# Kernel optimization log

Measured on AMD Instinct MI355X. Metric: run time of the kernel, lower is better.

Reference implementation:

```python
import jax, jax.numpy as jnp
import numpy as np

TAU = 0.2        # temperature
LAM = 0.5        # lambda_weight
P = 128          # proj_dim


def l2n(x):
    # tf.math.l2_normalize semantics: x / sqrt(max(sum(x^2), eps))
    return x / jnp.sqrt(jnp.maximum(jnp.sum(x * x, axis=-1, keepdims=True), 1e-12))


def global_head(feat, W1, b1, W2, b2):
    # GlobalAveragePooling2D -> Dense(2048, relu) -> Dense(128); dropout is identity in eval
    g = jnp.mean(feat, axis=(1, 2))                       # [B, C]
    return jax.nn.relu(g @ W1 + b1) @ W2 + b2             # [B, 128]


def dense_head(feat, W1, b1, W2, b2):
    # 1x1 Conv2D(2048, relu) -> 1x1 Conv2D(128) == per-pixel matmuls
    h = jax.nn.relu(jnp.einsum('bhwc,cd->bhwd', feat, W1) + b1)
    return jnp.einsum('bhwd,de->bhwe', h, W2) + b2        # [B, H, W, 128]


def dense_correspondence(q, k):
    b, h, w, c = q.shape
    f1 = q.reshape(b, h * w, c)
    f2 = k.reshape(b, h * w, c)
    sim = jnp.einsum('bnc,bmc->bnm', f1, f2)              # [B, hw, hw]
    idx = jnp.argmax(sim, axis=-1)                        # [B, hw]
    return jnp.take_along_axis(f2, idx[:, :, None], axis=1)  # batched gather


def info_nce(q, k):
    logits = (q @ k.T) / TAU                              # [N, N]
    lse = jax.nn.logsumexp(logits, axis=-1)
    pos = jnp.diagonal(logits)                            # labels = arange(N)
    return jnp.mean(lse - pos)


def queue_info_nce(q, k, queue):
    l_pos = jnp.sum(q * k, axis=-1, keepdims=True)        # [B, 1]
    l_neg = q @ queue.T                                   # [B, Q]
    logits = jnp.concatenate([l_pos, l_neg], axis=1) / TAU
    # labels are all zero -> positive logit is column 0
    return jnp.mean(jax.nn.logsumexp(logits, axis=-1) - logits[:, 0])


def setup_inputs() -> dict:
    key = jax.random.key(0)
    ks = jax.random.split(key, 16)
    B, H, W, C, D = 8, 28, 28, 1024, 2048
    Q = 65536
    s1 = 0.02
    inp = {
        'feat_q': jax.random.normal(ks[0], (B, H, W, C), jnp.float32),
        'feat_k': jax.random.normal(ks[1], (B, H, W, C), jnp.float32),
        'Wg1': jax.random.normal(ks[2], (C, D), jnp.float32) * s1,
        'bg1': jnp.zeros((D,), jnp.float32),
        'Wg2': jax.random.normal(ks[3], (D, P), jnp.float32) * s1,
        'bg2': jnp.zeros((P,), jnp.float32),
        'Wd1': jax.random.normal(ks[4], (C, D), jnp.float32) * s1,
        'bd1': jnp.zeros((D,), jnp.float32),
        'Wd2': jax.random.normal(ks[5], (D, P), jnp.float32) * s1,
        'bd2': jnp.zeros((P,), jnp.float32),
        'mWg1': jax.random.normal(ks[6], (C, D), jnp.float32) * s1,
        'mbg1': jnp.zeros((D,), jnp.float32),
        'mWg2': jax.random.normal(ks[7], (D, P), jnp.float32) * s1,
        'mbg2': jnp.zeros((P,), jnp.float32),
        'mWd1': jax.random.normal(ks[8], (C, D), jnp.float32) * s1,
        'mbd1': jnp.zeros((D,), jnp.float32),
        'mWd2': jax.random.normal(ks[9], (D, P), jnp.float32) * s1,
        'mbd2': jnp.zeros((P,), jnp.float32),
        'queue': l2n(jax.random.normal(ks[10], (Q, P), jnp.float32)),
    }
    return inp


def reference(feat_q, feat_k, Wg1, bg1, Wg2, bg2, Wd1, bd1, Wd2, bd2,
              mWg1, mbg1, mWg2, mbg2, mWd1, mbd1, mWd2, mbd2, queue):
    # student branch
    q_g = l2n(global_head(feat_q, Wg1, bg1, Wg2, bg2))
    q_d = l2n(dense_head(feat_q, Wd1, bd1, Wd2, bd2))
    # momentum (teacher) branch, stop-gradient as in train_step
    k_g = jax.lax.stop_gradient(l2n(global_head(feat_k, mWg1, mbg1, mWg2, mbg2)))
    k_d = jax.lax.stop_gradient(l2n(dense_head(feat_k, mWd1, mbd1, mWd2, mbd2)))
    # post-warmup path (warmup_epochs=0)
    l_g = queue_info_nce(q_g, k_g, queue)
    matched_k = dense_correspondence(q_d, k_d)
    l_d = info_nce(q_d.reshape(-1, P), matched_k.reshape(-1, P))
    total = (1.0 - LAM) * l_g + LAM * l_d
    return total
```

## Files before the change

kernel.cpp:

```cpp
#include <hip/hip_runtime.h>
#include <cstdint>

#define TAU_INV 5.0f
#define L2E 1.4426950408889634f

using ushort = unsigned short;
typedef __attribute__((ext_vector_type(8))) short s16x8;
typedef __attribute__((ext_vector_type(4))) float f32x4;

static __device__ __forceinline__ ushort f2bf(float x) {
  unsigned u = __float_as_uint(x);
  return (ushort)((u + 0x7fffu + ((u >> 16) & 1u)) >> 16);
}

static __device__ __forceinline__ float fexp2(float x) {
#if __has_builtin(__builtin_amdgcn_exp2f)
  return __builtin_amdgcn_exp2f(x);
#else
  return exp2f(x);
#endif
}

static __device__ __forceinline__ void gload_lds16(const void* g, void* l) {
  __builtin_amdgcn_global_load_lds(
      reinterpret_cast<const __attribute__((address_space(1))) void*>(
          reinterpret_cast<uintptr_t>(g)),
      reinterpret_cast<__attribute__((address_space(3))) void*>(
          (unsigned)reinterpret_cast<uintptr_t>(l)),
      16, 0, 0);
}

static __device__ __forceinline__ void xcd_swizzle(int gx, int gy, int& bx, int& by) {
  int nwg = gx * gy;
  int flat = by * gx + bx;
  int q = nwg >> 3, r = nwg & 7;
  int xcd = flat & 7, sl = flat >> 3;
  int tile = (xcd < r ? xcd * (q + 1) : r * (q + 1) + (xcd - r) * q) + sl;
  by = tile / gx;
  bx = tile - by * gx;
}

__global__ void k_cvt_pool(const float* __restrict__ fq, const float* __restrict__ fk,
                           ushort* __restrict__ obf, float* __restrict__ gpart) {
  int br = blockIdx.y >> 3, b = blockIdx.y & 7, pc = blockIdx.x, t = threadIdx.x;
  const float* feat = br ? fk : fq;
  const float* fp = feat + ((size_t)b * 784 + (size_t)pc * 7) * 1024;
  ushort* op = obf + (size_t)br * 6422528 + ((size_t)b * 784 + (size_t)pc * 7) * 1024;
  float4 acc = {0.f, 0.f, 0.f, 0.f};
#pragma unroll
  for (int p = 0; p < 7; ++p) {
    float4 v = ((const float4*)(fp + (size_t)p * 1024))[t];
    acc.x += v.x; acc.y += v.y; acc.z += v.z; acc.w += v.w;
    ushort4 r;
    r.x = f2bf(v.x); r.y = f2bf(v.y); r.z = f2bf(v.z); r.w = f2bf(v.w);
    ((ushort4*)(op + (size_t)p * 1024))[t] = r;
  }
  ((float4*)(gpart + ((size_t)blockIdx.y * 112 + pc) * 1024))[t] = acc;
}

__global__ void k_gpool_fin(const float* __restrict__ gpart, float* __restrict__ g) {
  int idx = blockIdx.x * 256 + threadIdx.x;
  int bb = idx >> 10, c = idx & 1023;
  float s = 0.f;
#pragma unroll 4
  for (int pc = 0; pc < 112; ++pc) s += gpart[((size_t)bb * 112 + pc) * 1024 + c];
  g[idx] = s * (1.0f / 784.0f);
}

__global__ void k_dense1_part(const float* __restrict__ g, const float* __restrict__ W0,
                              const float* __restrict__ W1, float* __restrict__ part1) {
  int br = blockIdx.z;
  const float* gb = g + (size_t)br * 8192;
  const float* W = br ? W1 : W0;
  float* p1 = part1 + (size_t)br * 262144;
  int d = blockIdx.x * 256 + threadIdx.x;
  int k0 = blockIdx.y * 64;
  __shared__ float gs[512];
  for (int i = threadIdx.x; i < 512; i += 256) gs[i] = gb[(i >> 6) * 1024 + k0 + (i & 63)];
  __syncthreads();
  float acc[8] = {};
  for (int kk = 0; kk < 64; ++kk) {
    float w = W[(size_t)(k0 + kk) * 2048 + d];
#pragma unroll
    for (int b = 0; b < 8; ++b) acc[b] += gs[b * 64 + kk] * w;
  }
#pragma unroll
  for (int b = 0; b < 8; ++b) p1[((size_t)blockIdx.y * 8 + b) * 2048 + d] = acc[b];
}

__global__ void k_d12(const float* __restrict__ part1, const float* __restrict__ b10,
                      const float* __restrict__ b11, const float* __restrict__ W20,
                      const float* __restrict__ W21, float* __restrict__ part2) {
  int br = blockIdx.y, k0 = blockIdx.x * 64;
  const float* p1 = part1 + (size_t)br * 262144;
  const float* b1 = br ? b11 : b10;
  const float* W2 = br ? W21 : W20;
  float* p2 = part2 + (size_t)br * 32768;
  __shared__ float hs[512];
  for (int i = threadIdx.x; i < 512; i += 128) {
    int b = i >> 6, kk = i & 63;
    float s = b1[k0 + kk];
#pragma unroll
    for (int ks = 0; ks < 16; ++ks) s += p1[((size_t)ks * 8 + b) * 2048 + k0 + kk];
    hs[i] = fmaxf(s, 0.f);
  }
  __syncthreads();
  int d = threadIdx.x;
  float acc[8] = {};
  for (int kk = 0; kk < 64; ++kk) {
    float w = W2[(size_t)(k0 + kk) * 128 + d];
#pragma unroll
    for (int b = 0; b < 8; ++b) acc[b] += hs[b * 64 + kk] * w;
  }
#pragma unroll
  for (int b = 0; b < 8; ++b) p2[((size_t)blockIdx.x * 8 + b) * 128 + d] = acc[b];
}

__global__ void k_head_fin(const float* __restrict__ p2q, const float* __restrict__ p2k,
                           const float* __restrict__ bq, const float* __restrict__ bk,
                           float* __restrict__ qg, float* __restrict__ kg,
                           float* __restrict__ lpos) {
  int b = blockIdx.x, lane = threadIdx.x;
  float q0 = bq[lane], q1 = bq[lane + 64];
  float k0 = bk[lane], k1 = bk[lane + 64];
#pragma unroll
  for (int s = 0; s < 32; ++s) {
    size_t base = ((size_t)s * 8 + b) * 128;
    q0 += p2q[base + lane]; q1 += p2q[base + lane + 64];
    k0 += p2k[base + lane]; k1 += p2k[base + lane + 64];
  }
  float sq = q0 * q0 + q1 * q1, sk = k0 * k0 + k1 * k1;
#pragma unroll
  for (int d = 1; d < 64; d <<= 1) { sq += __shfl_xor(sq, d); sk += __shfl_xor(sk, d); }
  float rq = 1.0f / sqrtf(fmaxf(sq, 1e-12f));
  float rk = 1.0f / sqrtf(fmaxf(sk, 1e-12f));
  q0 *= rq; q1 *= rq; k0 *= rk; k1 *= rk;
  qg[b * 128 + lane] = q0; qg[b * 128 + 64 + lane] = q1;
  kg[b * 128 + lane] = k0; kg[b * 128 + 64 + lane] = k1;
  float lp = q0 * k0 + q1 * k1;
#pragma unroll
  for (int d = 1; d < 64; d <<= 1) lp += __shfl_xor(lp, d);
  if (lane == 0) lpos[b] = lp;
}

__global__ void k_transpose_cvt(const float* __restrict__ W0, const float* __restrict__ W1,
                                ushort* __restrict__ Wt, int K, int N, size_t strideOut) {
  const float* W = blockIdx.z ? W1 : W0;
  ushort* o = Wt + (size_t)blockIdx.z * strideOut;
  __shared__ float tile[32][33];
  int n0 = blockIdx.x * 32, k0 = blockIdx.y * 32;
  int tx = threadIdx.x & 31, ty = threadIdx.x >> 5;
#pragma unroll
  for (int i = 0; i < 32; i += 8)
    tile[ty + i][tx] = W[(size_t)(k0 + ty + i) * N + n0 + tx];
  __syncthreads();
#pragma unroll
  for (int i = 0; i < 32; i += 8)
    o[(size_t)(n0 + ty + i) * K + k0 + tx] = f2bf(tile[tx][ty + i]);
}

__global__ __launch_bounds__(256) void k_gemm_e1(
    const ushort* __restrict__ A, long sA, const ushort* __restrict__ B, long sB,
    const float* __restrict__ bias0, const float* __restrict__ bias1,
    ushort* __restrict__ O, long sO, int K, int ldOut) {
  __shared__ unsigned char smem[65536];
  const int tid = threadIdx.x;
  int bx = blockIdx.x, by = blockIdx.y;
  const int bz = blockIdx.z;
  xcd_swizzle(gridDim.x, gridDim.y, bx, by);
  const ushort* Ab = A + (size_t)bz * sA;
  const ushort* Bb = B + (size_t)bz * sB;
  const float* bias = bz ? bias1 : bias0;
  ushort* Ob = O + (size_t)bz * sO;
  const int mBase = by * 128, nBase = bx * 128;
  const int lane = tid & 63;
  const int wid = tid >> 6;
  const int wid_u = __builtin_amdgcn_readfirstlane(wid);
  const int wm = wid >> 1, wn = wid & 1;
  const int lg = lane >> 4, li = lane & 15;
  const int lrow = lane >> 3, lchunk = lane & 7;

  const ushort* aSrc[4];
  const ushort* bSrc[4];
  int ldsOff[4];
#pragma unroll
  for (int j = 0; j < 4; ++j) {
    int r = wid_u * 32 + j * 8 + lrow;
    int gc = (lchunk ^ lrow) << 3;
    aSrc[j] = Ab + (size_t)(mBase + r) * K + gc;
    bSrc[j] = Bb + (size_t)(nBase + r) * K + gc;
    ldsOff[j] = (wid_u * 32 + j * 8) * 128;
  }
  f32x4 acc[4][4] = {};

  auto STAGE = [&](int buf, int k0) {
    unsigned base = (unsigned)buf * 32768u;
#pragma unroll
    for (int j = 0; j < 4; ++j) {
      gload_lds16(aSrc[j] + k0, smem + base + ldsOff[j]);
      gload_lds16(bSrc[j] + k0, smem + base + 16384 + ldsOff[j]);
    }
  };

  const int nt = K >> 6;
  STAGE(0, 0);
  __syncthreads();
  for (int t = 0; t < nt; ++t) {
    if (t + 1 < nt) STAGE((t + 1) & 1, (t + 1) << 6);
    const unsigned char* As = smem + (t & 1) * 32768;
    const unsigned char* Bs = As + 16384;
#pragma unroll
    for (int ks = 0; ks < 2; ++ks) {
      s16x8 af[4], bfr[4];
#pragma unroll
      for (int mi = 0; mi < 4; ++mi) {
        int r = wm * 64 + mi * 16 + li;
        af[mi] = *(const s16x8*)(const void*)(As + r * 128 + ((ks * 64 + lg * 16) ^ ((r & 7) << 4)));
      }
#pragma unroll
      for (int ni = 0; ni < 4; ++ni) {
        int c = wn * 64 + ni * 16 + li;
        bfr[ni] = *(const s16x8*)(const void*)(Bs + c * 128 + ((ks * 64 + lg * 16) ^ ((c & 7) << 4)));
      }
#pragma unroll
      for (int mi = 0; mi < 4; ++mi)
#pragma unroll
        for (int ni = 0; ni < 4; ++ni)
          acc[mi][ni] = __builtin_amdgcn_mfma_f32_16x16x32_bf16(af[mi], bfr[ni], acc[mi][ni], 0, 0, 0);
    }
    __syncthreads();
  }

#pragma unroll
  for (int ni = 0; ni < 4; ++ni) {
    int c = nBase + wn * 64 + ni * 16 + li;
    float bv = bias[c];
#pragma unroll
    for (int mi = 0; mi < 4; ++mi) {
#pragma unroll
      for (int rg = 0; rg < 4; ++rg) {
        int r = mBase + wm * 64 + mi * 16 + lg * 4 + rg;
        float v = fmaxf(acc[mi][ni][rg] + bv, 0.f);
        Ob[(size_t)r * ldOut + c] = f2bf(v);
      }
    }
  }
}

template <int EPI>
__global__ __launch_bounds__(256) void k_gemm_abt(
    const ushort* __restrict__ A, const ushort* __restrict__ B,
    const float* __restrict__ bias, void* __restrict__ o0, void* __restrict__ o1,
    int Mvalid, int Nvalid, int Kloop, int lda, int ldb, int ldOut, int ntiles,
    float scale, long sA, long sB) {
  __shared__ unsigned char smem[65536];
  const int tid = threadIdx.x;
  int bx = blockIdx.x, by = blockIdx.y;
  const int bz = blockIdx.z;
  xcd_swizzle(gridDim.x, gridDim.y, bx, by);
  const ushort* Ab;
  const ushort* Bb;
  if constexpr (EPI == 4) {
    Ab = A + (size_t)(bz >> 2) * sA + (size_t)(bz & 3) * Kloop;
    Bb = B + (size_t)(bz >> 2) * sB + (size_t)(bz & 3) * Kloop;
  } else {
    Ab = A + (size_t)bz * sA;
    Bb = B + (size_t)bz * sB;
  }
  const int mBase = by * 128, nBase = bx * 128;
  const int lane = tid & 63;
  const int wid = tid >> 6;
  const int wid_u = __builtin_amdgcn_readfirstlane(wid);
  const int wm = wid >> 1, wn = wid & 1;
  const int lg = lane >> 4, li = lane & 15;
  const int lrow = lane >> 3, lchunk = lane & 7;

  const ushort* aSrc[4];
  const ushort* bSrc[4];
  int ldsOff[4];
#pragma unroll
  for (int j = 0; j < 4; ++j) {
    int r = wid_u * 32 + j * 8 + lrow;
    int gc = (lchunk ^ lrow) << 3;
    int ga = mBase + r; ga = ga < Mvalid ? ga : Mvalid - 1;
    int gb = nBase + r; gb = gb < Nvalid ? gb : Nvalid - 1;
    aSrc[j] = Ab + (size_t)ga * lda + gc;
    bSrc[j] = Bb + (size_t)gb * ldb + gc;
    ldsOff[j] = (wid_u * 32 + j * 8) * 128;
  }
  f32x4 acc[4][4] = {};

  auto STAGE = [&](int buf, int k0) {
    unsigned base = (unsigned)buf * 32768u;
#pragma unroll
    for (int j = 0; j < 4; ++j) {
      gload_lds16(aSrc[j] + k0, smem + base + ldsOff[j]);
      gload_lds16(bSrc[j] + k0, smem + base + 16384 + ldsOff[j]);
    }
  };

  const int nt = Kloop >> 6;
  STAGE(0, 0);
  __syncthreads();
  for (int t = 0; t < nt; ++t) {
    if (t + 1 < nt) STAGE((t + 1) & 1, (t + 1) << 6);
    const unsigned char* As = smem + (t & 1) * 32768;
    const unsigned char* Bs = As + 16384;
#pragma unroll
    for (int ks = 0; ks < 2; ++ks) {
      s16x8 af[4], bfr[4];
#pragma unroll
      for (int mi = 0; mi < 4; ++mi) {
        int r = wm * 64 + mi * 16 + li;
        af[mi] = *(const s16x8*)(const void*)(As + r * 128 + ((ks * 64 + lg * 16) ^ ((r & 7) << 4)));
      }
#pragma unroll
      for (int ni = 0; ni < 4; ++ni) {
        int c = wn * 64 + ni * 16 + li;
        bfr[ni] = *(const s16x8*)(const void*)(Bs + c * 128 + ((ks * 64 + lg * 16) ^ ((c & 7) << 4)));
      }
#pragma unroll
      for (int mi = 0; mi < 4; ++mi)
#pragma unroll
        for (int ni = 0; ni < 4; ++ni)
          acc[mi][ni] = __builtin_amdgcn_mfma_f32_16x16x32_bf16(af[mi], bfr[ni], acc[mi][ni], 0, 0, 0);
    }
    __syncthreads();
  }

  if constexpr (EPI == 4) {
#pragma unroll
    for (int ni = 0; ni < 4; ++ni) {
      int c = nBase + wn * 64 + ni * 16 + li;
#pragma unroll
      for (int mi = 0; mi < 4; ++mi)
#pragma unroll
        for (int rg = 0; rg < 4; ++rg) {
          int r = mBase + wm * 64 + mi * 16 + lg * 4 + rg;
          if (r < Mvalid && c < Nvalid)
            ((float*)o0)[(size_t)bz * ntiles + (size_t)r * ldOut + c] = acc[mi][ni][rg];
        }
    }
  } else if constexpr (EPI == 2) {
    __syncthreads();
    float* reds = (float*)(void*)smem;
#pragma unroll
    for (int mi = 0; mi < 4; ++mi)
#pragma unroll
      for (int rg = 0; rg < 4; ++rg) {
        float s = fexp2(acc[mi][0][rg] * scale) + fexp2(acc[mi][1][rg] * scale) +
                  fexp2(acc[mi][2][rg] * scale) + fexp2(acc[mi][3][rg] * scale);
#pragma unroll
        for (int d = 1; d < 16; d <<= 1) s += __shfl_xor(s, d);
        int rl = wm * 64 + mi * 16 + lg * 4 + rg;
        if (li == 0) reds[rl * 2 + wn] = s;
      }
    __syncthreads();
    if (tid < 128) {
      size_t idx = (size_t)(mBase + tid) * ntiles + bx;
      ((float*)o0)[idx] = reds[tid * 2] + reds[tid * 2 + 1];
    }
  } else if constexpr (EPI == 3) {
    __syncthreads();
    float* redv = (float*)(void*)smem;
    int* redi = (int*)(void*)(smem + 1024);
#pragma unroll
    for (int mi = 0; mi < 4; ++mi)
#pragma unroll
      for (int rg = 0; rg < 4; ++rg) {
        float bv = -3.4e38f;
        int bi = 0x7fffffff;
#pragma unroll
        for (int ni = 0; ni < 4; ++ni) {
          int c = nBase + wn * 64 + ni * 16 + li;
          float v = (c < Nvalid) ? acc[mi][ni][rg] : -3.4e38f;
          if (v > bv || (v == bv && c < bi)) { bv = v; bi = c; }
        }
#pragma unroll
        for (int d = 1; d < 16; d <<= 1) {
          float ov = __shfl_xor(bv, d);
          int oi = __shfl_xor(bi, d);
          if (ov > bv || (ov == bv && oi < bi)) { bv = ov; bi = oi; }
        }
        int rl = wm * 64 + mi * 16 + lg * 4 + rg;
        if (li == 0) { redv[rl * 2 + wn] = bv; redi[rl * 2 + wn] = bi; }
      }
    __syncthreads();
    if (tid < 128) {
      int r = mBase + tid;
      if (r < Mvalid) {
        float v0 = redv[tid * 2], v1 = redv[tid * 2 + 1];
        int i0 = redi[tid * 2], i1 = redi[tid * 2 + 1];
        float v = v0; int bi2 = i0;
        if (v1 > v || (v1 == v && i1 < bi2)) { v = v1; bi2 = i1; }
        size_t idx = (size_t)(bz * Mvalid + r) * ntiles + bx;
        ((float*)o0)[idx] = v;
        ((int*)o1)[idx] = bi2;
      }
    }
  }
}

__global__ void k_l2n_rows(const float* __restrict__ part, const float* __restrict__ bias0,
                           const float* __restrict__ bias1, float* __restrict__ of,
                           ushort* __restrict__ ob) {
  int br = blockIdx.y;
  const float* p = part + (size_t)br * 3211264;
  const float* bias = br ? bias1 : bias0;
  float* o = of + (size_t)br * 802816;
  ushort* o2 = ob + (size_t)br * 802816;
  int row = blockIdx.x * 4 + (threadIdx.x >> 6);
  int lane = threadIdx.x & 63;
  size_t i0 = (size_t)row * 128 + lane;
  const size_t SL = 802816;
  float v0 = bias[lane]      + p[i0]      + p[SL + i0]      + p[2 * SL + i0]      + p[3 * SL + i0];
  float v1 = bias[lane + 64] + p[i0 + 64] + p[SL + i0 + 64] + p[2 * SL + i0 + 64] + p[3 * SL + i0 + 64];
  float ss = v0 * v0 + v1 * v1;
#pragma unroll
  for (int d = 1; d < 64; d <<= 1) ss += __shfl_xor(ss, d);
  float r = 1.0f / sqrtf(fmaxf(ss, 1e-12f));
  o[i0] = v0 * r;
  o[i0 + 64] = v1 * r;
  o2[i0] = f2bf(v0 * r);
  o2[i0 + 64] = f2bf(v1 * r);
}

__global__ void k_argmax_gather(const float* __restrict__ pval, const int* __restrict__ pidx,
                                const ushort* __restrict__ kd_bf, ushort* __restrict__ matched_bf,
                                int* __restrict__ idxf) {
  int n = blockIdx.x;
  int b = n / 784;
  float bv = pval[(size_t)n * 7];
  int bi = pidx[(size_t)n * 7];
#pragma unroll
  for (int t = 1; t < 7; ++t) {
    float v = pval[(size_t)n * 7 + t];
    int i2 = pidx[(size_t)n * 7 + t];
    if (v > bv) { bv = v; bi = i2; }
  }
  int lane = threadIdx.x;
  if (lane == 0) idxf[n] = bi;
  const ushort* src = kd_bf + (size_t)(b * 784 + bi) * 128;
  ushort* dst = matched_bf + (size_t)n * 128;
  dst[lane] = src[lane];
  dst[lane + 64] = src[lane + 64];
}

__global__ __launch_bounds__(256) void k_queue_nce(const float* __restrict__ queue,
                                                   const float* __restrict__ qg,
                                                   float* __restrict__ ps) {
  __shared__ float qs[1024];
  int tid = threadIdx.x;
  for (int i = tid; i < 1024; i += 256) qs[i] = qg[i];
  __syncthreads();
  int r = blockIdx.x * 256 + tid;
  const float* qr = queue + (size_t)r * 128;
  float a[8] = {0, 0, 0, 0, 0, 0, 0, 0};
  for (int j = 0; j < 128; j += 4) {
    float4 v = *(const float4*)(const void*)(qr + j);
#pragma unroll
    for (int b = 0; b < 8; ++b)
      a[b] += v.x * qs[b * 128 + j] + v.y * qs[b * 128 + j + 1] +
              v.z * qs[b * 128 + j + 2] + v.w * qs[b * 128 + j + 3];
  }
  __shared__ float lssum[8][4];
  int lane = tid & 63, w = tid >> 6;
#pragma unroll
  for (int b = 0; b < 8; ++b) {
    float s = fexp2(a[b] * (TAU_INV * L2E));
#pragma unroll
    for (int d = 1; d < 64; d <<= 1) s += __shfl_xor(s, d);
    if (lane == 0) lssum[b][w] = s;
  }
  __syncthreads();
  if (tid < 8) {
    int b = tid;
    ps[blockIdx.x * 8 + b] = lssum[b][0] + lssum[b][1] + lssum[b][2] + lssum[b][3];
  }
}

__global__ void k_row_lse(const float* __restrict__ psum, const int* __restrict__ idxf,
                          const float* __restrict__ qd, const float* __restrict__ kd,
                          float* __restrict__ diff) {
  int n = blockIdx.x * 4 + (threadIdx.x >> 6);
  int lane = threadIdx.x & 63;
  float s = (lane < 49) ? psum[(size_t)n * 49 + lane] : 0.f;
#pragma unroll
  for (int d = 1; d < 64; d <<= 1) s += __shfl_xor(s, d);
  int b = n / 784;
  int mr = b * 784 + idxf[n];
  float pos = qd[(size_t)n * 128 + lane] * kd[(size_t)mr * 128 + lane] +
              qd[(size_t)n * 128 + 64 + lane] * kd[(size_t)mr * 128 + 64 + lane];
#pragma unroll
  for (int d = 1; d < 64; d <<= 1) pos += __shfl_xor(pos, d);
  if (lane == 0) diff[n] = logf(s) - pos * TAU_INV;
}

__global__ void k_final(const float* __restrict__ ps, const float* __restrict__ lpos,
                        const float* __restrict__ diff, float* __restrict__ out) {
  int tid = threadIdx.x;
  int lane = tid & 63, w = tid >> 6;
  __shared__ float sm[4];
  float lg = 0.f;
  for (int b = 0; b < 8; ++b) {
    float s = ps[tid * 8 + b];
#pragma unroll
    for (int d = 1; d < 64; d <<= 1) s += __shfl_xor(s, d);
    if (lane == 0) sm[w] = s;
    __syncthreads();
    if (tid == 0) {
      float S = sm[0] + sm[1] + sm[2] + sm[3];
      float lp = lpos[b] * TAU_INV;
      S += fexp2(lp * L2E);
      lg += logf(S) - lp;
    }
    __syncthreads();
  }
  float v = 0.f;
  for (int i = tid; i < 6272; i += 256) v += diff[i];
#pragma unroll
  for (int d = 1; d < 64; d <<= 1) v += __shfl_xor(v, d);
  if (lane == 0) sm[w] = v;
  __syncthreads();
  if (tid == 0) {
    float ld = sm[0] + sm[1] + sm[2] + sm[3];
    out[0] = 0.5f * (lg * 0.125f) + 0.5f * (ld * (1.0f / 6272.0f));
  }
}

extern "C" void kernel_launch(void* const* d_in, const int* in_sizes, int n_in,
                              void* d_out, int out_size, void* d_ws, size_t ws_size,
                              hipStream_t stream) {
  (void)in_sizes; (void)n_in; (void)out_size; (void)ws_size;
  const float* feat_q = (const float*)d_in[0];
  const float* feat_k = (const float*)d_in[1];
  const float* Wg1 = (const float*)d_in[2];
  const float* bg1 = (const float*)d_in[3];
  const float* Wg2 = (const float*)d_in[4];
  const float* bg2 = (const float*)d_in[5];
  const float* Wd1 = (const float*)d_in[6];
  const float* bd1 = (const float*)d_in[7];
  const float* Wd2 = (const float*)d_in[8];
  const float* bd2 = (const float*)d_in[9];
  const float* mWg1 = (const float*)d_in[10];
  const float* mbg1 = (const float*)d_in[11];
  const float* mWg2 = (const float*)d_in[12];
  const float* mbg2 = (const float*)d_in[13];
  const float* mWd1 = (const float*)d_in[14];
  const float* mbd1 = (const float*)d_in[15];
  const float* mWd2 = (const float*)d_in[16];
  const float* mbd2 = (const float*)d_in[17];
  const float* queue = (const float*)d_in[18];
  float* out = (float*)d_out;

  char* ws = (char*)d_ws;
  size_t off = 0;
  auto alloc = [&](size_t bytes) -> void* {
    void* p = (void*)(ws + off);
    off += (bytes + 255) & ~(size_t)255;
    return p;
  };

  ushort* feat_bf = (ushort*)alloc(2ull * 6272 * 1024 * 2);
  ushort* Wd1t2 = (ushort*)alloc(2ull * 2048 * 1024 * 2);
  ushort* Wd2t2 = (ushort*)alloc(2ull * 128 * 2048 * 2);
  ushort* h_bf2 = (ushort*)alloc(2ull * 6272 * 2048 * 2);
  float* e2part2 = (float*)alloc(2ull * 4 * 6272 * 128 * 4);
  float* qdkd = (float*)alloc(2ull * 6272 * 128 * 4);
  ushort* qdkd_bf = (ushort*)alloc(2ull * 6272 * 128 * 2);
  ushort* matched_bf = (ushort*)alloc(6272ull * 128 * 2);
  float* psum = (float*)alloc(6272ull * 49 * 4);
  float* pval = (float*)alloc(6272ull * 7 * 4);
  int* pidx = (int*)alloc(6272ull * 7 * 4);
  int* idxf = (int*)alloc(6272ull * 4);
  float* gpart = (float*)alloc(16ull * 112 * 1024 * 4);
  float* g2 = (float*)alloc(2ull * 8 * 1024 * 4);
  float* part1 = (float*)alloc(2ull * 16 * 8 * 2048 * 4);
  float* part2 = (float*)alloc(2ull * 32 * 8 * 128 * 4);
  float* qg = (float*)alloc(8ull * 128 * 4);
  float* kg = (float*)alloc(8ull * 128 * 4);
  float* l_pos = (float*)alloc(8ull * 4);
  float* qpart_s = (float*)alloc(256ull * 8 * 4);
  float* diff = (float*)alloc(6272ull * 4);

  k_cvt_pool<<<dim3(112, 16), 256, 0, stream>>>(feat_q, feat_k, feat_bf, gpart);
  k_gpool_fin<<<64, 256, 0, stream>>>(gpart, g2);

  k_transpose_cvt<<<dim3(64, 32, 2), 256, 0, stream>>>(Wd1, mWd1, Wd1t2, 1024, 2048, 2097152);
  k_transpose_cvt<<<dim3(4, 64, 2), 256, 0, stream>>>(Wd2, mWd2, Wd2t2, 2048, 128, 262144);

  k_dense1_part<<<dim3(8, 16, 2), 256, 0, stream>>>(g2, Wg1, mWg1, part1);
  k_d12<<<dim3(32, 2), 128, 0, stream>>>(part1, bg1, mbg1, Wg2, mWg2, part2);
  k_head_fin<<<8, 64, 0, stream>>>(part2, part2 + 32768, bg2, mbg2, qg, kg, l_pos);

  k_gemm_e1<<<dim3(16, 49, 2), 256, 0, stream>>>(feat_bf, 6422528, Wd1t2, 2097152,
                                                 bd1, mbd1, h_bf2, 12845056, 1024, 2048);
  k_gemm_abt<4><<<dim3(1, 49, 8), 256, 0, stream>>>(h_bf2, Wd2t2, nullptr, e2part2, nullptr,
                                                    6272, 128, 512, 2048, 2048, 128, 802816,
                                                    0.f, 12845056, 262144);
  k_l2n_rows<<<dim3(1568, 2), 256, 0, stream>>>(e2part2, bd2, mbd2, qdkd, qdkd_bf);

  k_gemm_abt<3><<<dim3(7, 7, 8), 256, 0, stream>>>(qdkd_bf, qdkd_bf + 802816, nullptr, pval, pidx,
                                                   784, 784, 128, 128, 128, 0, 7, 0.f,
                                                   784l * 128, 784l * 128);
  k_argmax_gather<<<6272, 64, 0, stream>>>(pval, pidx, qdkd_bf + 802816, matched_bf, idxf);

  k_gemm_abt<2><<<dim3(49, 49, 1), 256, 0, stream>>>(qdkd_bf, matched_bf, nullptr, psum, nullptr,
                                                     6272, 6272, 128, 128, 128, 0, 49,
                                                     TAU_INV * L2E, 0, 0);

  k_queue_nce<<<256, 256, 0, stream>>>(queue, qg, qpart_s);

  k_row_lse<<<1568, 256, 0, stream>>>(psum, idxf, qdkd, qdkd + 802816, diff);
  k_final<<<1, 256, 0, stream>>>(qpart_s, l_pos, diff, out);
}
```

Measured before the change: 230.8 us.

## Merge small launches and load K=128 GEMM fragments directly from global

Folds the two weight-transpose launches into one, and folds the queue-NCE and row-LSE kernels into one launch split by block index. This cuts kernel launch count and tail gaps. The K=128 similarity GEMMs (argmax and sum-exp) now read MFMA operands straight from global memory into registers instead of staging through double-buffered LDS, which removes LDS traffic and barriers. The trade-off is uncoalesced 16-byte fragment loads with no shared-memory reuse across waves. The K-split second projection GEMM is specialised with bounds clamps removed.

```diff
diff --git a/kernel.cpp b/kernel.cpp
--- a/kernel.cpp
+++ b/kernel.cpp
@@ -143,12 +143,25 @@
   if (lane == 0) lpos[b] = lp;
 }
 
-__global__ void k_transpose_cvt(const float* __restrict__ W0, const float* __restrict__ W1,
-                                ushort* __restrict__ Wt, int K, int N, size_t strideOut) {
-  const float* W = blockIdx.z ? W1 : W0;
-  ushort* o = Wt + (size_t)blockIdx.z * strideOut;
+__global__ void k_transpose_all(const float* __restrict__ Wd1, const float* __restrict__ mWd1,
+                                const float* __restrict__ Wd2, const float* __restrict__ mWd2,
+                                ushort* __restrict__ Wt1, ushort* __restrict__ Wt2) {
+  int fl = blockIdx.x, z = blockIdx.z;
+  const float* W;
+  ushort* o;
+  int bx, by, K, N;
+  if (fl < 2048) {
+    W = z ? mWd1 : Wd1;
+    o = Wt1 + (size_t)z * 2097152;
+    bx = fl & 63; by = fl >> 6; K = 1024; N = 2048;
+  } else {
+    fl -= 2048;
+    W = z ? mWd2 : Wd2;
+    o = Wt2 + (size_t)z * 262144;
+    bx = fl & 3; by = fl >> 2; K = 2048; N = 128;
+  }
   __shared__ float tile[32][33];
-  int n0 = blockIdx.x * 32, k0 = blockIdx.y * 32;
+  int n0 = bx * 32, k0 = by * 32;
   int tx = threadIdx.x & 31, ty = threadIdx.x >> 5;
 #pragma unroll
   for (int i = 0; i < 32; i += 8)
@@ -247,26 +260,16 @@
   }
 }
 
-template <int EPI>
-__global__ __launch_bounds__(256) void k_gemm_abt(
-    const ushort* __restrict__ A, const ushort* __restrict__ B,
-    const float* __restrict__ bias, void* __restrict__ o0, void* __restrict__ o1,
-    int Mvalid, int Nvalid, int Kloop, int lda, int ldb, int ldOut, int ntiles,
-    float scale, long sA, long sB) {
+__global__ __launch_bounds__(256) void k_gemm_e2(
+    const ushort* __restrict__ A, const ushort* __restrict__ B, float* __restrict__ o0,
+    int Kloop, int lda, int ldb, long sA, long sB) {
   __shared__ unsigned char smem[65536];
   const int tid = threadIdx.x;
   int bx = blockIdx.x, by = blockIdx.y;
   const int bz = blockIdx.z;
   xcd_swizzle(gridDim.x, gridDim.y, bx, by);
-  const ushort* Ab;
-  const ushort* Bb;
-  if constexpr (EPI == 4) {
-    Ab = A + (size_t)(bz >> 2) * sA + (size_t)(bz & 3) * Kloop;
-    Bb = B + (size_t)(bz >> 2) * sB + (size_t)(bz & 3) * Kloop;
-  } else {
-    Ab = A + (size_t)bz * sA;
-    Bb = B + (size_t)bz * sB;
-  }
+  const ushort* Ab = A + (size_t)(bz >> 2) * sA + (size_t)(bz & 3) * Kloop;
+  const ushort* Bb = B + (size_t)(bz >> 2) * sB + (size_t)(bz & 3) * Kloop;
   const int mBase = by * 128, nBase = bx * 128;
   const int lane = tid & 63;
   const int wid = tid >> 6;
@@ -282,10 +285,8 @@
   for (int j = 0; j < 4; ++j) {
     int r = wid_u * 32 + j * 8 + lrow;
     int gc = (lchunk ^ lrow) << 3;
-    int ga = mBase + r; ga = ga < Mvalid ? ga : Mvalid - 1;
-    int gb = nBase + r; gb = gb < Nvalid ? gb : Nvalid - 1;
-    aSrc[j] = Ab + (size_t)ga * lda + gc;
-    bSrc[j] = Bb + (size_t)gb * ldb + gc;
+    aSrc[j] = Ab + (size_t)(mBase + r) * lda + gc;
+    bSrc[j] = Bb + (size_t)(nBase + r) * ldb + gc;
     ldsOff[j] = (wid_u * 32 + j * 8) * 128;
   }
   f32x4 acc[4][4] = {};
@@ -328,21 +329,64 @@
     __syncthreads();
   }
 
-  if constexpr (EPI == 4) {
-#pragma unroll
-    for (int ni = 0; ni < 4; ++ni) {
-      int c = nBase + wn * 64 + ni * 16 + li;
-#pragma unroll
-      for (int mi = 0; mi < 4; ++mi)
-#pragma unroll
-        for (int rg = 0; rg < 4; ++rg) {
-          int r = mBase + wm * 64 + mi * 16 + lg * 4 + rg;
-          if (r < Mvalid && c < Nvalid)
-            ((float*)o0)[(size_t)bz * ntiles + (size_t)r * ldOut + c] = acc[mi][ni][rg];
-        }
-    }
-  } else if constexpr (EPI == 2) {
-    __syncthreads();
+#pragma unroll
+  for (int ni = 0; ni < 4; ++ni) {
+    int c = nBase + wn * 64 + ni * 16 + li;
+#pragma unroll
+    for (int mi = 0; mi < 4; ++mi)
+#pragma unroll
+      for (int rg = 0; rg < 4; ++rg) {
+        int r = mBase + wm * 64 + mi * 16 + lg * 4 + rg;
+        o0[(size_t)bz * 802816 + (size_t)r * 128 + c] = acc[mi][ni][rg];
+      }
+  }
+}
+
+template <int EPI>
+__global__ __launch_bounds__(256) void k_gemm_k128(
+    const ushort* __restrict__ A, const ushort* __restrict__ B,
+    float* __restrict__ o0, int* __restrict__ o1,
+    int Mvalid, int Nvalid, int ntiles, float scale, long sA, long sB) {
+  __shared__ unsigned char smem[2048];
+  const int tid = threadIdx.x;
+  int bx = blockIdx.x, by = blockIdx.y;
+  const int bz = blockIdx.z;
+  xcd_swizzle(gridDim.x, gridDim.y, bx, by);
+  const ushort* Ab = A + (size_t)bz * sA;
+  const ushort* Bb = B + (size_t)bz * sB;
+  const int mBase = by * 128, nBase = bx * 128;
+  const int lane = tid & 63;
+  const int wid = tid >> 6;
+  const int wm = wid >> 1, wn = wid & 1;
+  const int lg = lane >> 4, li = lane & 15;
+
+  s16x8 af[4][2], bfr[4][2];
+#pragma unroll
+  for (int mi = 0; mi < 4; ++mi) {
+    int r = mBase + wm * 64 + mi * 16 + li;
+    r = r < Mvalid ? r : Mvalid - 1;
+#pragma unroll
+    for (int ks = 0; ks < 2; ++ks)
+      af[mi][ks] = *(const s16x8*)(const void*)(Ab + (size_t)r * 128 + ks * 32 + lg * 8);
+  }
+#pragma unroll
+  for (int ni = 0; ni < 4; ++ni) {
+    int c = nBase + wn * 64 + ni * 16 + li;
+    c = c < Nvalid ? c : Nvalid - 1;
+#pragma unroll
+    for (int ks = 0; ks < 2; ++ks)
+      bfr[ni][ks] = *(const s16x8*)(const void*)(Bb + (size_t)c * 128 + ks * 32 + lg * 8);
+  }
+  f32x4 acc[4][4] = {};
+#pragma unroll
+  for (int ks = 0; ks < 2; ++ks)
+#pragma unroll
+    for (int mi = 0; mi < 4; ++mi)
+#pragma unroll
+      for (int ni = 0; ni < 4; ++ni)
+        acc[mi][ni] = __builtin_amdgcn_mfma_f32_16x16x32_bf16(af[mi][ks], bfr[ni][ks], acc[mi][ni], 0, 0, 0);
+
+  if constexpr (EPI == 2) {
     float* reds = (float*)(void*)smem;
 #pragma unroll
     for (int mi = 0; mi < 4; ++mi)
@@ -358,10 +402,9 @@
     __syncthreads();
     if (tid < 128) {
       size_t idx = (size_t)(mBase + tid) * ntiles + bx;
-      ((float*)o0)[idx] = reds[tid * 2] + reds[tid * 2 + 1];
-    }
-  } else if constexpr (EPI == 3) {
-    __syncthreads();
+      o0[idx] = reds[tid * 2] + reds[tid * 2 + 1];
+    }
+  } else {
     float* redv = (float*)(void*)smem;
     int* redi = (int*)(void*)(smem + 1024);
 #pragma unroll
@@ -394,8 +437,8 @@
         float v = v0; int bi2 = i0;
         if (v1 > v || (v1 == v && i1 < bi2)) { v = v1; bi2 = i1; }
         size_t idx = (size_t)(bz * Mvalid + r) * ntiles + bx;
-        ((float*)o0)[idx] = v;
-        ((int*)o1)[idx] = bi2;
+        o0[idx] = v;
+        o1[idx] = bi2;
       }
     }
   }
@@ -446,54 +489,56 @@
   dst[lane + 64] = src[lane + 64];
 }
 
-__global__ __launch_bounds__(256) void k_queue_nce(const float* __restrict__ queue,
-                                                   const float* __restrict__ qg,
-                                                   float* __restrict__ ps) {
+__global__ __launch_bounds__(256) void k_qrow(const float* __restrict__ queue,
+                                              const float* __restrict__ qg,
+                                              float* __restrict__ ps,
+                                              const float* __restrict__ psum,
+                                              const int* __restrict__ idxf,
+                                              const float* __restrict__ qd,
+                                              const float* __restrict__ kd,
+                                              float* __restrict__ diff) {
   __shared__ float qs[1024];
+  __shared__ float lssum[8][4];
   int tid = threadIdx.x;
-  for (int i = tid; i < 1024; i += 256) qs[i] = qg[i];
-  __syncthreads();
-  int r = blockIdx.x * 256 + tid;
-  const float* qr = queue + (size_t)r * 128;
-  float a[8] = {0, 0, 0, 0, 0, 0, 0, 0};
-  for (int j = 0; j < 128; j += 4) {
-    float4 v = *(const float4*)(const void*)(qr + j);
-#pragma unroll
-    for (int b = 0; b < 8; ++b)
-      a[b] += v.x * qs[b * 128 + j] + v.y * qs[b * 128 + j + 1] +
-              v.z * qs[b * 128 + j + 2] + v.w * qs[b * 128 + j + 3];
-  }
-  __shared__ float lssum[8][4];
   int lane = tid & 63, w = tid >> 6;
-#pragma unroll
-  for (int b = 0; b < 8; ++b) {
-    float s = fexp2(a[b] * (TAU_INV * L2E));
+  if (blockIdx.x < 256) {
+    for (int i = tid; i < 1024; i += 256) qs[i] = qg[i];
+    __syncthreads();
+    int r = blockIdx.x * 256 + tid;
+    const float* qr = queue + (size_t)r * 128;
+    float a[8] = {0, 0, 0, 0, 0, 0, 0, 0};
+    for (int j = 0; j < 128; j += 4) {
+      float4 v = *(const float4*)(const void*)(qr + j);
+#pragma unroll
+      for (int b = 0; b < 8; ++b)
+        a[b] += v.x * qs[b * 128 + j] + v.y * qs[b * 128 + j + 1] +
+                v.z * qs[b * 128 + j + 2] + v.w * qs[b * 128 + j + 3];
+    }
+#pragma unroll
+    for (int b = 0; b < 8; ++b) {
+      float s = fexp2(a[b] * (TAU_INV * L2E));
+#pragma unroll
+      for (int d = 1; d < 64; d <<= 1) s += __shfl_xor(s, d);
+      if (lane == 0) lssum[b][w] = s;
+    }
+    __syncthreads();
+    if (tid < 8) {
+      int b = tid;
+      ps[blockIdx.x * 8 + b] = lssum[b][0] + lssum[b][1] + lssum[b][2] + lssum[b][3];
+    }
+  } else {
+    int n = (blockIdx.x - 256) * 4 + w;
+    float s = (lane < 49) ? psum[(size_t)n * 49 + lane] : 0.f;
 #pragma unroll
     for (int d = 1; d < 64; d <<= 1) s += __shfl_xor(s, d);
-    if (lane == 0) lssum[b][w] = s;
-  }
-  __syncthreads();
-  if (tid < 8) {
-    int b = tid;
-    ps[blockIdx.x * 8 + b] = lssum[b][0] + lssum[b][1] + lssum[b][2] + lssum[b][3];
-  }
-}
-
-__global__ void k_row_lse(const float* __restrict__ psum, const int* __restrict__ idxf,
-                          const float* __restrict__ qd, const float* __restrict__ kd,
-                          float* __restrict__ diff) {
-  int n = blockIdx.x * 4 + (threadIdx.x >> 6);
-  int lane = threadIdx.x & 63;
-  float s = (lane < 49) ? psum[(size_t)n * 49 + lane] : 0.f;
-#pragma unroll
-  for (int d = 1; d < 64; d <<= 1) s += __shfl_xor(s, d);
-  int b = n / 784;
-  int mr = b * 784 + idxf[n];
-  float pos = qd[(size_t)n * 128 + lane] * kd[(size_t)mr * 128 + lane] +
-              qd[(size_t)n * 128 + 64 + lane] * kd[(size_t)mr * 128 + 64 + lane];
-#pragma unroll
-  for (int d = 1; d < 64; d <<= 1) pos += __shfl_xor(pos, d);
-  if (lane == 0) diff[n] = logf(s) - pos * TAU_INV;
+    int b = n / 784;
+    int mr = b * 784 + idxf[n];
+    float pos = qd[(size_t)n * 128 + lane] * kd[(size_t)mr * 128 + lane] +
+                qd[(size_t)n * 128 + 64 + lane] * kd[(size_t)mr * 128 + 64 + lane];
+#pragma unroll
+    for (int d = 1; d < 64; d <<= 1) pos += __shfl_xor(pos, d);
+    if (lane == 0) diff[n] = logf(s) - pos * TAU_INV;
+  }
 }
 
 __global__ void k_final(const float* __restrict__ ps, const float* __restrict__ lpos,
@@ -586,8 +631,7 @@
   k_cvt_pool<<<dim3(112, 16), 256, 0, stream>>>(feat_q, feat_k, feat_bf, gpart);
   k_gpool_fin<<<64, 256, 0, stream>>>(gpart, g2);
 
-  k_transpose_cvt<<<dim3(64, 32, 2), 256, 0, stream>>>(Wd1, mWd1, Wd1t2, 1024, 2048, 2097152);
-  k_transpose_cvt<<<dim3(4, 64, 2), 256, 0, stream>>>(Wd2, mWd2, Wd2t2, 2048, 128, 262144);
+  k_transpose_all<<<dim3(2304, 1, 2), 256, 0, stream>>>(Wd1, mWd1, Wd2, mWd2, Wd1t2, Wd2t2);
 
   k_dense1_part<<<dim3(8, 16, 2), 256, 0, stream>>>(g2, Wg1, mWg1, part1);
   k_d12<<<dim3(32, 2), 128, 0, stream>>>(part1, bg1, mbg1, Wg2, mWg2, part2);
@@ -595,22 +639,17 @@
 
   k_gemm_e1<<<dim3(16, 49, 2), 256, 0, stream>>>(feat_bf, 6422528, Wd1t2, 2097152,
                                                  bd1, mbd1, h_bf2, 12845056, 1024, 2048);
-  k_gemm_abt<4><<<dim3(1, 49, 8), 256, 0, stream>>>(h_bf2, Wd2t2, nullptr, e2part2, nullptr,
-                                                    6272, 128, 512, 2048, 2048, 128, 802816,
-                                                    0.f, 12845056, 262144);
+  k_gemm_e2<<<dim3(1, 49, 8), 256, 0, stream>>>(h_bf2, Wd2t2, e2part2,
+                                                512, 2048, 2048, 12845056, 262144);
   k_l2n_rows<<<dim3(1568, 2), 256, 0, stream>>>(e2part2, bd2, mbd2, qdkd, qdkd_bf);
 
-  k_gemm_abt<3><<<dim3(7, 7, 8), 256, 0, stream>>>(qdkd_bf, qdkd_bf + 802816, nullptr, pval, pidx,
-                                                   784, 784, 128, 128, 128, 0, 7, 0.f,
-                                                   784l * 128, 784l * 128);
+  k_gemm_k128<3><<<dim3(7, 7, 8), 256, 0, stream>>>(qdkd_bf, qdkd_bf + 802816, pval, pidx,
+                                                    784, 784, 7, 0.f, 784l * 128, 784l * 128);
   k_argmax_gather<<<6272, 64, 0, stream>>>(pval, pidx, qdkd_bf + 802816, matched_bf, idxf);
 
-  k_gemm_abt<2><<<dim3(49, 49, 1), 256, 0, stream>>>(qdkd_bf, matched_bf, nullptr, psum, nullptr,
-                                                     6272, 6272, 128, 128, 128, 0, 49,
-                                                     TAU_INV * L2E, 0, 0);
-
-  k_queue_nce<<<256, 256, 0, stream>>>(queue, qg, qpart_s);
-
-  k_row_lse<<<1568, 256, 0, stream>>>(psum, idxf, qdkd, qdkd + 802816, diff);
+  k_gemm_k128<2><<<dim3(49, 49, 1), 256, 0, stream>>>(qdkd_bf, matched_bf, psum, nullptr,
+                                                      6272, 6272, 49, TAU_INV * L2E, 0, 0);
+
+  k_qrow<<<1824, 256, 0, stream>>>(queue, qg, qpart_s, psum, idxf, qdkd, qdkd + 802816, diff);
   k_final<<<1, 256, 0, stream>>>(qpart_s, l_pos, diff, out);
 }
```

Result: faster. 219.0 us (-5.1%).
